# Kernel tuning notes

Hardware: AMD Instinct MI355X
Metric: run time of the kernel (lower is better)

Reference implementation:

```python
import jax, jax.numpy as jnp
import numpy as np
import math

B, T, D, H, FF = 2, 2048, 1024, 16, 4096
DH = D // H
EPS = 1e-5

def _ternary(key, out_f, in_f):
    # TFLELayer: ternary-quantized linear weight in {-1,0,1} (stored as f32 here)
    return jax.random.randint(key, (out_f, in_f), -1, 2).astype(jnp.float32)

def setup_inputs() -> dict:
    key = jax.random.key(0)
    ks = jax.random.split(key, 8)
    x = jax.random.normal(ks[0], (B, T, D), dtype=jnp.float32)
    mask = jnp.triu(jnp.ones((T, T), dtype=bool), k=1)  # True = masked (causal)
    return {
        "x": x,
        "mask": mask,
        "ln1_g": jnp.ones((D,), jnp.float32), "ln1_b": jnp.zeros((D,), jnp.float32),
        "ln2_g": jnp.ones((D,), jnp.float32), "ln2_b": jnp.zeros((D,), jnp.float32),
        "Wq": _ternary(ks[1], D, D), "Wk": _ternary(ks[2], D, D),
        "Wv": _ternary(ks[3], D, D), "Wo": _ternary(ks[4], D, D),
        "Wff1": _ternary(ks[5], FF, D), "Wff2": _ternary(ks[6], D, FF),
    }

def _ln(x, g, b):
    mu = jnp.mean(x, axis=-1, keepdims=True)
    var = jnp.var(x, axis=-1, keepdims=True)
    return (x - mu) * jax.lax.rsqrt(var + EPS) * g + b

def reference(x, mask, ln1_g, ln1_b, ln2_g, ln2_b, Wq, Wk, Wv, Wo, Wff1, Wff2):
    h = _ln(x, ln1_g, ln1_b)
    q = (h @ Wq.T).reshape(B, T, H, DH).transpose(0, 2, 1, 3)  # (B,H,T,DH)
    k = (h @ Wk.T).reshape(B, T, H, DH).transpose(0, 2, 1, 3)
    v = (h @ Wv.T).reshape(B, T, H, DH).transpose(0, 2, 1, 3)
    scale = 1.0 / math.sqrt(DH)
    attn = jnp.einsum('bhqd,bhkd->bhqk', q, k) * scale
    attn = jnp.where(mask[None, None], -jnp.inf, attn)
    attn = jax.nn.softmax(attn, axis=-1)
    out = jnp.einsum('bhqk,bhkd->bhqd', attn, v)
    out = out.transpose(0, 2, 1, 3).reshape(B, T, D) @ Wo.T
    x = x + out
    h = _ln(x, ln2_g, ln2_b)
    ff = jax.nn.gelu(h @ Wff1.T, approximate=False)
    ff = ff @ Wff2.T
    return x + ff
```

## Files before the change

### kernel.cpp

```cpp
#include <hip/hip_runtime.h>

typedef __bf16 bf16;
typedef bf16 bf16x8 __attribute__((ext_vector_type(8)));
typedef bf16 bf16x4 __attribute__((ext_vector_type(4)));
typedef float f32x4 __attribute__((ext_vector_type(4)));

static __device__ __forceinline__ void async16(const void* g, void* l) {
  __builtin_amdgcn_global_load_lds((__attribute__((address_space(1))) void*)g,
                                   (__attribute__((address_space(3))) void*)l,
                                   16, 0, 0);
}

__global__ __launch_bounds__(256) void cvt4(const float* __restrict__ a,
                                            const float* __restrict__ b,
                                            const float* __restrict__ c,
                                            const float* __restrict__ d,
                                            bf16* __restrict__ dst) {
  const size_t i = ((size_t)blockIdx.x * 256 + threadIdx.x) * 4;
  const size_t M1 = 1u << 20;
  const float* src = (i < M1) ? a : (i < 2 * M1) ? b : (i < 3 * M1) ? c : d;
  const size_t off = i & (M1 - 1);
  const float4 v = *(const float4*)(src + off);
  bf16x4 o = {(bf16)v.x, (bf16)v.y, (bf16)v.z, (bf16)v.w};
  *(bf16x4*)(dst + i) = o;
}

__global__ __launch_bounds__(256) void cvt2(const float* __restrict__ a,
                                            const float* __restrict__ b,
                                            bf16* __restrict__ dst) {
  const size_t i = ((size_t)blockIdx.x * 256 + threadIdx.x) * 4;
  const size_t M4 = 4u << 20;
  const float* src = (i < M4) ? a : b;
  const size_t off = (i < M4) ? i : i - M4;
  const float4 v = *(const float4*)(src + off);
  bf16x4 o = {(bf16)v.x, (bf16)v.y, (bf16)v.z, (bf16)v.w};
  *(bf16x4*)(dst + i) = o;
}

template <int EPI, bool SPLIT>
static __device__ __forceinline__ void gemm_body(
    const bf16* __restrict__ A, const bf16* __restrict__ A2,
    const bf16* __restrict__ B, void* __restrict__ Cv, void* __restrict__ C2,
    const float* __restrict__ R, float scale, int col0, int row0, int M, int N,
    int K) {
  __shared__ bf16 sA[128 * 32];
  __shared__ bf16 sB[128 * 32];
  const int tid = threadIdx.x;
  const int lane = tid & 63;
  const int wid = tid >> 6;
  const int wm = wid >> 1, wn = wid & 1;

  f32x4 acc[4][4];
  const f32x4 fzero = {0.f, 0.f, 0.f, 0.f};
#pragma unroll
  for (int i = 0; i < 4; ++i)
#pragma unroll
    for (int j = 0; j < 4; ++j) acc[i][j] = fzero;

  const int nk = K >> 5;
  const int total = SPLIT ? (nk << 1) : nk;
  const int r0 = tid >> 2, c0 = (tid & 3) << 3;
  const int r1 = (256 + tid) >> 2, c1 = ((256 + tid) & 3) << 3;
  bf16* lA0 = sA + (wid << 6) * 8;
  bf16* lA1 = sA + (256 + (wid << 6)) * 8;
  bf16* lB0 = sB + (wid << 6) * 8;
  bf16* lB1 = sB + (256 + (wid << 6)) * 8;

  for (int kt = 0; kt < total; ++kt) {
    const int kk = (kt < nk) ? kt : kt - nk;
    const bf16* Ap = (SPLIT && kt >= nk) ? A2 : A;
    const int k0 = kk << 5;
    async16(Ap + (size_t)(row0 + r0) * K + k0 + c0, lA0);
    async16(Ap + (size_t)(row0 + r1) * K + k0 + c1, lA1);
    async16(B + (size_t)(col0 + r0) * K + k0 + c0, lB0);
    async16(B + (size_t)(col0 + r1) * K + k0 + c1, lB1);
    __syncthreads();
    const int fr = lane & 15, fq = (lane >> 4) << 3;
    bf16x8 af[4], bfr[4];
#pragma unroll
    for (int i = 0; i < 4; ++i)
      af[i] = *(const bf16x8*)&sA[(wm * 64 + i * 16 + fr) * 32 + fq];
#pragma unroll
    for (int j = 0; j < 4; ++j)
      bfr[j] = *(const bf16x8*)&sB[(wn * 64 + j * 16 + fr) * 32 + fq];
#pragma unroll
    for (int i = 0; i < 4; ++i)
#pragma unroll
      for (int j = 0; j < 4; ++j)
        acc[i][j] = __builtin_amdgcn_mfma_f32_16x16x32_bf16(af[i], bfr[j],
                                                            acc[i][j], 0, 0, 0);
    __syncthreads();
  }

  const int fr = lane & 15, fq4 = (lane >> 4) << 2;
#pragma unroll
  for (int i = 0; i < 4; ++i) {
#pragma unroll
    for (int j = 0; j < 4; ++j) {
      const int rbase = row0 + wm * 64 + i * 16 + fq4;
      const int col = col0 + wn * 64 + j * 16 + fr;
      if constexpr (EPI == 5) {
        const int b = rbase >> 11, t = rbase & 2047;
        const int hh = col >> 6, d = col & 63;
        bf16x4 o4 = {(bf16)acc[i][j][0], (bf16)acc[i][j][1],
                     (bf16)acc[i][j][2], (bf16)acc[i][j][3]};
        *(bf16x4*)&((bf16*)Cv)[(((size_t)(b * 16 + hh)) * 64 + d) * 2048 + t] =
            o4;
      } else {
#pragma unroll
        for (int r = 0; r < 4; ++r) {
          const size_t idx = (size_t)(rbase + r) * N + col;
          const float val = acc[i][j][r];
          if constexpr (EPI == 0) {
            ((float*)Cv)[idx] = val;
          } else if constexpr (EPI == 2) {
            ((float*)Cv)[idx] = val + R[idx];
          } else if constexpr (EPI == 3) {
            ((bf16*)Cv)[idx] =
                (bf16)(0.5f * val * (1.0f + erff(val * 0.7071067811865476f)));
          } else {
            const float vs = val * scale;
            const bf16 hi = (bf16)vs;
            ((bf16*)Cv)[idx] = hi;
            ((bf16*)C2)[idx] = (bf16)(vs - (float)hi);
          }
        }
      }
    }
  }
}

template <int EPI, bool SPLIT>
__global__ __launch_bounds__(256) void gemm_bt(
    const bf16* __restrict__ A, const bf16* __restrict__ A2,
    const bf16* __restrict__ B, void* __restrict__ Cv,
    const float* __restrict__ R, int M, int N, int K) {
  gemm_body<EPI, SPLIT>(A, A2, B, Cv, nullptr, R, 1.0f, blockIdx.x * 128,
                        blockIdx.y * 128, M, N, K);
}

template <int EPI>
__global__ __launch_bounds__(256) void gemm_bt64(
    const bf16* __restrict__ A, const bf16* __restrict__ B,
    void* __restrict__ Cv, const float* __restrict__ R, int M, int N, int K) {
  __shared__ bf16 sA[128 * 32];
  __shared__ bf16 sB[64 * 32];
  const int col0 = blockIdx.x * 64, row0 = blockIdx.y * 128;
  const int tid = threadIdx.x;
  const int lane = tid & 63;
  const int wid = tid >> 6;
  const int wm = wid >> 1, wn = wid & 1;

  f32x4 acc[4][2];
  const f32x4 fzero = {0.f, 0.f, 0.f, 0.f};
#pragma unroll
  for (int i = 0; i < 4; ++i)
#pragma unroll
    for (int j = 0; j < 2; ++j) acc[i][j] = fzero;

  const int nk = K >> 5;
  const int r0 = tid >> 2, c0 = (tid & 3) << 3;
  const int r1 = (256 + tid) >> 2, c1 = ((256 + tid) & 3) << 3;
  bf16* lA0 = sA + (wid << 6) * 8;
  bf16* lA1 = sA + (256 + (wid << 6)) * 8;
  bf16* lB0 = sB + (wid << 6) * 8;

  for (int kt = 0; kt < nk; ++kt) {
    const int k0 = kt << 5;
    async16(A + (size_t)(row0 + r0) * K + k0 + c0, lA0);
    async16(A + (size_t)(row0 + r1) * K + k0 + c1, lA1);
    async16(B + (size_t)(col0 + r0) * K + k0 + c0, lB0);
    __syncthreads();
    const int fr = lane & 15, fq = (lane >> 4) << 3;
    bf16x8 af[4], bfr[2];
#pragma unroll
    for (int i = 0; i < 4; ++i)
      af[i] = *(const bf16x8*)&sA[(wm * 64 + i * 16 + fr) * 32 + fq];
#pragma unroll
    for (int j = 0; j < 2; ++j)
      bfr[j] = *(const bf16x8*)&sB[(wn * 32 + j * 16 + fr) * 32 + fq];
#pragma unroll
    for (int i = 0; i < 4; ++i)
#pragma unroll
      for (int j = 0; j < 2; ++j)
        acc[i][j] = __builtin_amdgcn_mfma_f32_16x16x32_bf16(af[i], bfr[j],
                                                            acc[i][j], 0, 0, 0);
    __syncthreads();
  }

  const int fr = lane & 15, fq4 = (lane >> 4) << 2;
#pragma unroll
  for (int i = 0; i < 4; ++i) {
#pragma unroll
    for (int j = 0; j < 2; ++j) {
      const int rbase = row0 + wm * 64 + i * 16 + fq4;
      const int col = col0 + wn * 32 + j * 16 + fr;
#pragma unroll
      for (int r = 0; r < 4; ++r) {
        const size_t idx = (size_t)(rbase + r) * N + col;
        const float val = acc[i][j][r];
        if constexpr (EPI == 2) {
          ((float*)Cv)[idx] = val + R[idx];
        } else {
          ((float*)Cv)[idx] = val;
        }
      }
    }
  }
}

__global__ __launch_bounds__(256) void gemm_qkv(
    const bf16* __restrict__ A, const bf16* __restrict__ A2,
    const bf16* __restrict__ Bq, const bf16* __restrict__ Bk,
    const bf16* __restrict__ Bv, bf16* qh, bf16* ql, bf16* kh, bf16* kl,
    bf16* vt) {
  const int which = blockIdx.x >> 3;
  const int col0 = (blockIdx.x & 7) * 128, row0 = blockIdx.y * 128;
  if (which == 2) {
    gemm_body<5, false>(A, nullptr, Bv, (void*)vt, nullptr, nullptr, 1.0f,
                        col0, row0, 4096, 1024, 1024);
  } else {
    gemm_body<4, true>(A, A2, which ? Bk : Bq, which ? (void*)kh : (void*)qh,
                       which ? (void*)kl : (void*)ql, nullptr,
                       which ? 1.0f : 0.125f, col0, row0, 4096, 1024, 1024);
  }
}

template <bool SPLIT>
__global__ __launch_bounds__(256) void ln_kernel(
    const float* __restrict__ x, const float* __restrict__ g,
    const float* __restrict__ b, bf16* __restrict__ hi, bf16* __restrict__ lo) {
  const int row = blockIdx.x;
  const int tid = threadIdx.x;
  const float* xr = x + (size_t)row * 1024;
  float v[4];
  float s1 = 0.f, s2 = 0.f;
#pragma unroll
  for (int j = 0; j < 4; ++j) {
    v[j] = xr[j * 256 + tid];
    s1 += v[j];
    s2 += v[j] * v[j];
  }
#pragma unroll
  for (int off = 1; off < 64; off <<= 1) {
    s1 += __shfl_xor(s1, off);
    s2 += __shfl_xor(s2, off);
  }
  __shared__ float ws1[4], ws2[4];
  const int wid = tid >> 6;
  if ((tid & 63) == 0) {
    ws1[wid] = s1;
    ws2[wid] = s2;
  }
  __syncthreads();
  s1 = ws1[0] + ws1[1] + ws1[2] + ws1[3];
  s2 = ws2[0] + ws2[1] + ws2[2] + ws2[3];
  const float mu = s1 * (1.f / 1024.f);
  const float var = s2 * (1.f / 1024.f) - mu * mu;
  const float rstd = 1.0f / sqrtf(var + 1e-5f);
#pragma unroll
  for (int j = 0; j < 4; ++j) {
    const int cc = j * 256 + tid;
    const float y = (v[j] - mu) * rstd * g[cc] + b[cc];
    const bf16 yh = (bf16)y;
    hi[(size_t)row * 1024 + cc] = yh;
    if constexpr (SPLIT) lo[(size_t)row * 1024 + cc] = (bf16)(y - (float)yh);
  }
}

__global__ __launch_bounds__(256) void attn_kernel(
    const bf16* __restrict__ qh_g, const bf16* __restrict__ ql_g,
    const bf16* __restrict__ kh_g, const bf16* __restrict__ kl_g,
    const bf16* __restrict__ vt_g, bf16* __restrict__ out) {
  __shared__ bf16 lds[18688];
  bf16* Kh = lds;
  bf16* Kl = lds + 4608;
  bf16* Vt = lds + 9216;
  bf16* Ps = lds + 13824;

  const int bid = blockIdx.x;
  const int qt = 31 - (bid >> 5);
  const int h = bid & 15;
  const int b = (bid >> 4) & 1;
  const int t0 = qt << 6;
  const int tid = threadIdx.x;
  const int w = tid >> 6;
  const int lane = tid & 63;
  const int c = lane & 15;
  const int quad = lane >> 4;

  const int r0 = tid >> 3, c0 = (tid & 7) << 3;
  const int r1 = (tid + 256) >> 3, c1 = ((tid + 256) & 7) << 3;

  const size_t qrow =
      ((size_t)(b * 2048 + t0 + w * 16 + c)) * 1024 + h * 64 + quad * 8;
  bf16x8 aqh[2], aql[2];
  aqh[0] = *(const bf16x8*)&qh_g[qrow];
  aqh[1] = *(const bf16x8*)&qh_g[qrow + 32];
  aql[0] = *(const bf16x8*)&ql_g[qrow];
  aql[1] = *(const bf16x8*)&ql_g[qrow + 32];

  f32x4 o[4];
  const f32x4 fzero = {0.f, 0.f, 0.f, 0.f};
#pragma unroll
  for (int j = 0; j < 4; ++j) o[j] = fzero;
  float m_i[4] = {-3e38f, -3e38f, -3e38f, -3e38f};
  float l_i[4] = {0.f, 0.f, 0.f, 0.f};

  const size_t vtb = ((size_t)(b * 16 + h)) * 64 * 2048;
  const size_t kband = ((size_t)(b * 2048)) * 1024 + h * 64;

  bf16x8 gk[6];
  {
    gk[0] = *(const bf16x8*)&kh_g[kband + (size_t)r0 * 1024 + c0];
    gk[1] = *(const bf16x8*)&kh_g[kband + (size_t)r1 * 1024 + c1];
    gk[2] = *(const bf16x8*)&kl_g[kband + (size_t)r0 * 1024 + c0];
    gk[3] = *(const bf16x8*)&kl_g[kband + (size_t)r1 * 1024 + c1];
    gk[4] = *(const bf16x8*)&vt_g[vtb + (size_t)r0 * 2048 + c0];
    gk[5] = *(const bf16x8*)&vt_g[vtb + (size_t)r1 * 2048 + c1];
  }

  for (int kt = 0; kt <= qt; ++kt) {
    __syncthreads();
    *(bf16x8*)&Kh[r0 * 72 + c0] = gk[0];
    *(bf16x8*)&Kh[r1 * 72 + c1] = gk[1];
    *(bf16x8*)&Kl[r0 * 72 + c0] = gk[2];
    *(bf16x8*)&Kl[r1 * 72 + c1] = gk[3];
    *(bf16x8*)&Vt[r0 * 72 + c0] = gk[4];
    *(bf16x8*)&Vt[r1 * 72 + c1] = gk[5];
    __syncthreads();

    if (kt < qt) {
      const int kb1 = (kt + 1) << 6;
      const size_t kbase = kband + (size_t)kb1 * 1024;
      gk[0] = *(const bf16x8*)&kh_g[kbase + (size_t)r0 * 1024 + c0];
      gk[1] = *(const bf16x8*)&kh_g[kbase + (size_t)r1 * 1024 + c1];
      gk[2] = *(const bf16x8*)&kl_g[kbase + (size_t)r0 * 1024 + c0];
      gk[3] = *(const bf16x8*)&kl_g[kbase + (size_t)r1 * 1024 + c1];
      gk[4] = *(const bf16x8*)&vt_g[vtb + (size_t)r0 * 2048 + kb1 + c0];
      gk[5] = *(const bf16x8*)&vt_g[vtb + (size_t)r1 * 2048 + kb1 + c1];
    }

    bf16x8 bkh[4][2], bkl[4][2];
#pragma unroll
    for (int j = 0; j < 4; ++j)
#pragma unroll
      for (int s = 0; s < 2; ++s) {
        bkh[j][s] = *(const bf16x8*)&Kh[(j * 16 + c) * 72 + s * 32 + quad * 8];
        bkl[j][s] = *(const bf16x8*)&Kl[(j * 16 + c) * 72 + s * 32 + quad * 8];
      }

    f32x4 s4[4];
#pragma unroll
    for (int j = 0; j < 4; ++j) s4[j] = fzero;
#pragma unroll
    for (int j = 0; j < 4; ++j)
#pragma unroll
      for (int s = 0; s < 2; ++s) {
        s4[j] = __builtin_amdgcn_mfma_f32_16x16x32_bf16(aqh[s], bkh[j][s], s4[j], 0, 0, 0);
        s4[j] = __builtin_amdgcn_mfma_f32_16x16x32_bf16(aqh[s], bkl[j][s], s4[j], 0, 0, 0);
        s4[j] = __builtin_amdgcn_mfma_f32_16x16x32_bf16(aql[s], bkh[j][s], s4[j], 0, 0, 0);
      }

    if (kt == qt) {
#pragma unroll
      for (int j = 0; j < 4; ++j)
#pragma unroll
        for (int r = 0; r < 4; ++r)
          if (j * 16 + c > w * 16 + quad * 4 + r) s4[j][r] = -3e38f;
    }

    float al[4], p[4][4];
#pragma unroll
    for (int r = 0; r < 4; ++r) {
      float mt = fmaxf(fmaxf(s4[0][r], s4[1][r]), fmaxf(s4[2][r], s4[3][r]));
#pragma unroll
      for (int off = 1; off < 16; off <<= 1) mt = fmaxf(mt, __shfl_xor(mt, off));
      const float mn = fmaxf(m_i[r], mt);
      al[r] = __expf(m_i[r] - mn);
      float ps = 0.f;
#pragma unroll
      for (int j = 0; j < 4; ++j) {
        p[r][j] = __expf(s4[j][r] - mn);
        ps += p[r][j];
      }
#pragma unroll
      for (int off = 1; off < 16; off <<= 1) ps += __shfl_xor(ps, off);
      l_i[r] = l_i[r] * al[r] + ps;
      m_i[r] = mn;
#pragma unroll
      for (int j = 0; j < 4; ++j) o[j][r] *= al[r];
    }

    bf16* Pw = Ps + w * 16 * 76;
#pragma unroll
    for (int r = 0; r < 4; ++r)
#pragma unroll
      for (int j = 0; j < 4; ++j)
        Pw[(quad * 4 + r) * 76 + j * 16 + c] = (bf16)p[r][j];

    bf16x8 ap[2], bv[4][2];
#pragma unroll
    for (int s = 0; s < 2; ++s)
      ap[s] = *(const bf16x8*)&Pw[c * 76 + s * 32 + quad * 8];
#pragma unroll
    for (int j = 0; j < 4; ++j)
#pragma unroll
      for (int s = 0; s < 2; ++s)
        bv[j][s] = *(const bf16x8*)&Vt[(j * 16 + c) * 72 + s * 32 + quad * 8];
#pragma unroll
    for (int j = 0; j < 4; ++j)
#pragma unroll
      for (int s = 0; s < 2; ++s)
        o[j] = __builtin_amdgcn_mfma_f32_16x16x32_bf16(ap[s], bv[j][s], o[j], 0, 0, 0);
  }

#pragma unroll
  for (int r = 0; r < 4; ++r) {
    const float inv = 1.0f / l_i[r];
#pragma unroll
    for (int j = 0; j < 4; ++j) {
      const size_t oi =
          ((size_t)(b * 2048 + t0 + w * 16 + quad * 4 + r)) * 1024 + h * 64 +
          j * 16 + c;
      out[oi] = (bf16)(o[j][r] * inv);
    }
  }
}

extern "C" void kernel_launch(void* const* d_in, const int* in_sizes, int n_in,
                              void* d_out, int out_size, void* d_ws,
                              size_t ws_size, hipStream_t stream) {
  const float* x = (const float*)d_in[0];
  const float* g1 = (const float*)d_in[2];
  const float* b1 = (const float*)d_in[3];
  const float* g2 = (const float*)d_in[4];
  const float* b2 = (const float*)d_in[5];
  const float* Wq = (const float*)d_in[6];
  const float* Wk = (const float*)d_in[7];
  const float* Wv = (const float*)d_in[8];
  const float* Wo = (const float*)d_in[9];
  const float* Wf1 = (const float*)d_in[10];
  const float* Wf2 = (const float*)d_in[11];
  char* ws = (char*)d_ws;
  const size_t MB = 1024 * 1024;
  const size_t M1 = 1u << 20;
  bf16* Wq_b = (bf16*)ws;
  bf16* Wk_b = Wq_b + 1 * M1;
  bf16* Wv_b = Wq_b + 2 * M1;
  bf16* Wo_b = Wq_b + 3 * M1;
  bf16* h_hi = (bf16*)(ws + 8 * MB);
  bf16* h_lo = (bf16*)(ws + 16 * MB);
  bf16* Wf1_b = h_hi;
  bf16* Wf2_b = h_lo;
  bf16* qh = (bf16*)(ws + 24 * MB);
  bf16* ql = (bf16*)(ws + 32 * MB);
  bf16* kh = (bf16*)(ws + 40 * MB);
  bf16* kl = (bf16*)(ws + 48 * MB);
  bf16* vt = (bf16*)(ws + 56 * MB);
  bf16* attnout = (bf16*)(ws + 64 * MB);
  float* x1 = (float*)qh;
  bf16* h2 = (bf16*)(ws + 72 * MB);
  bf16* ff = kh;
  float* outp = (float*)d_out;

  cvt4<<<4096, 256, 0, stream>>>(Wq, Wk, Wv, Wo, Wq_b);
  ln_kernel<true><<<4096, 256, 0, stream>>>(x, g1, b1, h_hi, h_lo);
  gemm_qkv<<<dim3(24, 32), 256, 0, stream>>>(h_hi, h_lo, Wq_b, Wk_b, Wv_b, qh,
                                             ql, kh, kl, vt);
  cvt2<<<8192, 256, 0, stream>>>(Wf1, Wf2, Wf1_b);
  attn_kernel<<<1024, 256, 0, stream>>>(qh, ql, kh, kl, vt, attnout);
  gemm_bt64<2><<<dim3(16, 32), 256, 0, stream>>>(attnout, Wo_b, (void*)x1, x,
                                                 4096, 1024, 1024);
  ln_kernel<false><<<4096, 256, 0, stream>>>(x1, g2, b2, h2, nullptr);
  gemm_bt<3, false><<<dim3(32, 32), 256, 0, stream>>>(
      h2, nullptr, Wf1_b, (void*)ff, nullptr, 4096, 4096, 1024);
  gemm_bt64<2><<<dim3(16, 32), 256, 0, stream>>>(ff, Wf2_b, (void*)outp, x1,
                                                 4096, 1024, 4096);
}
```

Baseline: 470.6 us.

## Merge split-precision QKV GEMM loads and use DPP row reductions in attention

Adds a dedicated Q/K GEMM path that loads hi and lo A tiles together and runs both MFMAs per tile in one K loop, replacing the generic split gemm_body call. It also replaces the shfl_xor-based 16-lane max/sum reductions in the attention softmax with DPP row_ror reductions to avoid LDS-permute round trips. The merged GEMM uses more LDS and registers, which may lower occupancy. It keeps a single-stage load/sync loop with no double buffering.

```diff
diff --git a/kernel.cpp b/kernel.cpp
--- a/kernel.cpp
+++ b/kernel.cpp
@@ -9,6 +9,27 @@
   __builtin_amdgcn_global_load_lds((__attribute__((address_space(1))) void*)g,
                                    (__attribute__((address_space(3))) void*)l,
                                    16, 0, 0);
+}
+
+template <int N>
+static __device__ __forceinline__ float ror16(float x) {
+  const int y =
+      __builtin_amdgcn_update_dpp(0, __float_as_int(x), 0x120 | N, 0xf, 0xf, true);
+  return __int_as_float(y);
+}
+static __device__ __forceinline__ float rowmax16(float x) {
+  x = fmaxf(x, ror16<8>(x));
+  x = fmaxf(x, ror16<4>(x));
+  x = fmaxf(x, ror16<2>(x));
+  x = fmaxf(x, ror16<1>(x));
+  return x;
+}
+static __device__ __forceinline__ float rowsum16(float x) {
+  x += ror16<8>(x);
+  x += ror16<4>(x);
+  x += ror16<2>(x);
+  x += ror16<1>(x);
+  return x;
 }
 
 __global__ __launch_bounds__(256) void cvt4(const float* __restrict__ a,
@@ -139,6 +160,100 @@
                         blockIdx.y * 128, M, N, K);
 }
 
+static __device__ __forceinline__ void gemm_split_merged(
+    const bf16* __restrict__ A, const bf16* __restrict__ A2,
+    const bf16* __restrict__ B, bf16* __restrict__ Chi, bf16* __restrict__ Clo,
+    float scale, int col0, int row0) {
+  constexpr int K = 1024, N = 1024;
+  __shared__ bf16 sAh[128 * 32];
+  __shared__ bf16 sAl[128 * 32];
+  __shared__ bf16 sB[128 * 32];
+  const int tid = threadIdx.x;
+  const int lane = tid & 63;
+  const int wid = tid >> 6;
+  const int wm = wid >> 1, wn = wid & 1;
+
+  f32x4 acc[4][4];
+  const f32x4 fzero = {0.f, 0.f, 0.f, 0.f};
+#pragma unroll
+  for (int i = 0; i < 4; ++i)
+#pragma unroll
+    for (int j = 0; j < 4; ++j) acc[i][j] = fzero;
+
+  const int r0 = tid >> 2, c0 = (tid & 3) << 3;
+  const int r1 = (256 + tid) >> 2, c1 = ((256 + tid) & 3) << 3;
+  bf16* lAh0 = sAh + (wid << 6) * 8;
+  bf16* lAh1 = sAh + (256 + (wid << 6)) * 8;
+  bf16* lAl0 = sAl + (wid << 6) * 8;
+  bf16* lAl1 = sAl + (256 + (wid << 6)) * 8;
+  bf16* lB0 = sB + (wid << 6) * 8;
+  bf16* lB1 = sB + (256 + (wid << 6)) * 8;
+
+  for (int kt = 0; kt < 32; ++kt) {
+    const int k0 = kt << 5;
+    async16(A + (size_t)(row0 + r0) * K + k0 + c0, lAh0);
+    async16(A + (size_t)(row0 + r1) * K + k0 + c1, lAh1);
+    async16(A2 + (size_t)(row0 + r0) * K + k0 + c0, lAl0);
+    async16(A2 + (size_t)(row0 + r1) * K + k0 + c1, lAl1);
+    async16(B + (size_t)(col0 + r0) * K + k0 + c0, lB0);
+    async16(B + (size_t)(col0 + r1) * K + k0 + c1, lB1);
+    __syncthreads();
+    const int fr = lane & 15, fq = (lane >> 4) << 3;
+    bf16x8 ah[4], al[4], bfr[4];
+#pragma unroll
+    for (int i = 0; i < 4; ++i) {
+      ah[i] = *(const bf16x8*)&sAh[(wm * 64 + i * 16 + fr) * 32 + fq];
+      al[i] = *(const bf16x8*)&sAl[(wm * 64 + i * 16 + fr) * 32 + fq];
+    }
+#pragma unroll
+    for (int j = 0; j < 4; ++j)
+      bfr[j] = *(const bf16x8*)&sB[(wn * 64 + j * 16 + fr) * 32 + fq];
+#pragma unroll
+    for (int i = 0; i < 4; ++i)
+#pragma unroll
+      for (int j = 0; j < 4; ++j) {
+        acc[i][j] = __builtin_amdgcn_mfma_f32_16x16x32_bf16(ah[i], bfr[j],
+                                                            acc[i][j], 0, 0, 0);
+        acc[i][j] = __builtin_amdgcn_mfma_f32_16x16x32_bf16(al[i], bfr[j],
+                                                            acc[i][j], 0, 0, 0);
+      }
+    __syncthreads();
+  }
+
+  const int fr = lane & 15, fq4 = (lane >> 4) << 2;
+#pragma unroll
+  for (int i = 0; i < 4; ++i)
+#pragma unroll
+    for (int j = 0; j < 4; ++j) {
+      const int rbase = row0 + wm * 64 + i * 16 + fq4;
+      const int col = col0 + wn * 64 + j * 16 + fr;
+#pragma unroll
+      for (int r = 0; r < 4; ++r) {
+        const size_t idx = (size_t)(rbase + r) * N + col;
+        const float vs = acc[i][j][r] * scale;
+        const bf16 hi = (bf16)vs;
+        Chi[idx] = hi;
+        Clo[idx] = (bf16)(vs - (float)hi);
+      }
+    }
+}
+
+__global__ __launch_bounds__(256) void gemm_qkv(
+    const bf16* __restrict__ A, const bf16* __restrict__ A2,
+    const bf16* __restrict__ Bq, const bf16* __restrict__ Bk,
+    const bf16* __restrict__ Bv, bf16* qh, bf16* ql, bf16* kh, bf16* kl,
+    bf16* vt) {
+  const int which = blockIdx.x >> 3;
+  const int col0 = (blockIdx.x & 7) * 128, row0 = blockIdx.y * 128;
+  if (which == 2) {
+    gemm_body<5, false>(A, nullptr, Bv, (void*)vt, nullptr, nullptr, 1.0f,
+                        col0, row0, 4096, 1024, 1024);
+  } else {
+    gemm_split_merged(A, A2, which ? Bk : Bq, which ? kh : qh, which ? kl : ql,
+                      which ? 1.0f : 0.125f, col0, row0);
+  }
+}
+
 template <int EPI>
 __global__ __launch_bounds__(256) void gemm_bt64(
     const bf16* __restrict__ A, const bf16* __restrict__ B,
@@ -209,23 +324,6 @@
   }
 }
 
-__global__ __launch_bounds__(256) void gemm_qkv(
-    const bf16* __restrict__ A, const bf16* __restrict__ A2,
-    const bf16* __restrict__ Bq, const bf16* __restrict__ Bk,
-    const bf16* __restrict__ Bv, bf16* qh, bf16* ql, bf16* kh, bf16* kl,
-    bf16* vt) {
-  const int which = blockIdx.x >> 3;
-  const int col0 = (blockIdx.x & 7) * 128, row0 = blockIdx.y * 128;
-  if (which == 2) {
-    gemm_body<5, false>(A, nullptr, Bv, (void*)vt, nullptr, nullptr, 1.0f,
-                        col0, row0, 4096, 1024, 1024);
-  } else {
-    gemm_body<4, true>(A, A2, which ? Bk : Bq, which ? (void*)kh : (void*)qh,
-                       which ? (void*)kl : (void*)ql, nullptr,
-                       which ? 1.0f : 0.125f, col0, row0, 4096, 1024, 1024);
-  }
-}
-
 template <bool SPLIT>
 __global__ __launch_bounds__(256) void ln_kernel(
     const float* __restrict__ x, const float* __restrict__ g,
@@ -374,8 +472,7 @@
 #pragma unroll
     for (int r = 0; r < 4; ++r) {
       float mt = fmaxf(fmaxf(s4[0][r], s4[1][r]), fmaxf(s4[2][r], s4[3][r]));
-#pragma unroll
-      for (int off = 1; off < 16; off <<= 1) mt = fmaxf(mt, __shfl_xor(mt, off));
+      mt = rowmax16(mt);
       const float mn = fmaxf(m_i[r], mt);
       al[r] = __expf(m_i[r] - mn);
       float ps = 0.f;
@@ -384,8 +481,7 @@
         p[r][j] = __expf(s4[j][r] - mn);
         ps += p[r][j];
       }
-#pragma unroll
-      for (int off = 1; off < 16; off <<= 1) ps += __shfl_xor(ps, off);
+      ps = rowsum16(ps);
       l_i[r] = l_i[r] * al[r] + ps;
       m_i[r] = mn;
 #pragma unroll
```

Result: no change. 465.6 us (-1.1%).
